# Kernel tuning notes

Hardware: AMD Instinct MI355X
Metric: run time of the kernel (lower is better)

## Reference

```python
import jax, jax.numpy as jnp
import numpy as np

D_MODEL = 2048
NUM_HEADS = 32
HEAD_DIM = D_MODEL // NUM_HEADS  # 64
ROPE_BASE = 10000.0


def _rope_cos_sin(seq_len, head_dim, dtype):
    inv_freq = 1.0 / (ROPE_BASE ** (jnp.arange(0, head_dim, 2, dtype=jnp.float32) / head_dim))
    freqs = jnp.arange(seq_len, dtype=jnp.float32)[:, None] * inv_freq[None, :]  # (S, Dh/2)
    emb = jnp.concatenate([freqs, freqs], axis=-1)  # (S, Dh)
    return emb.astype(dtype), jnp.cos(emb).astype(dtype), jnp.sin(emb).astype(dtype)


def _rotate_half(x):
    x1, x2 = jnp.split(x, 2, axis=-1)
    return jnp.concatenate([-x2, x1], axis=-1)


def setup_inputs() -> dict:
    key = jax.random.key(0)
    k1, k2, k3, k4 = jax.random.split(key, 4)
    B, S, D = 1, 2048, D_MODEL
    x = jax.random.normal(k1, (B, S, D), dtype=jnp.float32)
    Wqkv = jax.random.normal(k2, (3 * D, D), dtype=jnp.float32) * 0.02
    Wo = jax.random.normal(k3, (D, D), dtype=jnp.float32) * 0.02
    gate = jax.random.normal(k4, (D,), dtype=jnp.float32) * 0.1
    return {"x": x, "Wqkv": Wqkv, "Wo": Wo, "gate": gate}


def reference(x, Wqkv, Wo, gate):
    B, S, D = x.shape
    H, Dh = NUM_HEADS, HEAD_DIM
    residual = x

    # fused QKV projection (torch Linear: y = x @ W.T)
    qkv = jnp.einsum('bsd,ed->bse', x, Wqkv).reshape(B, S, 3, H, Dh)
    q, k, v = qkv[:, :, 0], qkv[:, :, 1], qkv[:, :, 2]  # each (B, S, H, Dh)

    # RoPE
    _, cos, sin = _rope_cos_sin(S, Dh, x.dtype)
    cos = cos[None, :, None, :]  # (1, S, 1, Dh)
    sin = sin[None, :, None, :]
    q = q * cos + _rotate_half(q) * sin
    k = k * cos + _rotate_half(k) * sin

    # causal SDPA
    scale = 1.0 / np.sqrt(Dh)
    scores = jnp.einsum('bqhd,bkhd->bhqk', q, k) * scale  # (B, H, S, S)
    causal = jnp.tril(jnp.ones((S, S), dtype=bool))
    scores = jnp.where(causal[None, None], scores, jnp.finfo(scores.dtype).min)
    probs = jax.nn.softmax(scores, axis=-1)
    attn = jnp.einsum('bhqk,bkhd->bqhd', probs, v).reshape(B, S, D)

    out = jnp.einsum('bsd,ed->bse', attn, Wo)
    # HeoGate: learned per-channel gated residual (assumption; see notes)
    return residual + gate * out
```

## Files before the change

### kernel.cpp

```cpp
#include <hip/hip_runtime.h>
#include <hip/hip_bf16.h>
#include <cstdint>
#include <cstddef>

typedef __hip_bfloat16 bf16;
typedef short short8 __attribute__((ext_vector_type(8)));
typedef float f32x4 __attribute__((ext_vector_type(4)));

#define S_LEN 2048
#define DMODEL 2048
#define NQKV 6144
#define NHEADS 32
#define HDIM 64
#define ROPE_L2 0.4152410118609203f

__device__ __forceinline__ void async_copy16(const bf16* g, bf16* l) {
  __builtin_amdgcn_global_load_lds(
      (const __attribute__((address_space(1))) void*)g,
      (__attribute__((address_space(3))) void*)l, 16, 0, 0);
}

__device__ __forceinline__ f32x4 mfma_bf16(short8 a, short8 b, f32x4 c) {
  return __builtin_amdgcn_mfma_f32_16x16x32_bf16(a, b, c, 0, 0, 0);
}

__global__ __launch_bounds__(256) void cvt3_kernel(const float* __restrict__ sx,
                                                   bf16* __restrict__ dx,
                                                   const float* __restrict__ sw,
                                                   bf16* __restrict__ dw,
                                                   const float* __restrict__ so,
                                                   bf16* __restrict__ dov) {
  int i = blockIdx.x * 256 + threadIdx.x;
  const float* s;
  bf16* d;
  if (i < 1048576) {
    s = sx; d = dx;
  } else if (i < 4194304) {
    s = sw; d = dw; i -= 1048576;
  } else {
    s = so; d = dov; i -= 4194304;
  }
  const float4 v = ((const float4*)s)[i];
  union { bf16 h[4]; ushort4 u; } tmp;
  tmp.h[0] = __float2bfloat16(v.x);
  tmp.h[1] = __float2bfloat16(v.y);
  tmp.h[2] = __float2bfloat16(v.z);
  tmp.h[3] = __float2bfloat16(v.w);
  ((ushort4*)d)[i] = tmp.u;
}

#define QKV_NT 32
#define QBAR() do { __builtin_amdgcn_s_barrier(); __builtin_amdgcn_sched_barrier(0); } while (0)
#define WAITV(n) asm volatile("s_waitcnt vmcnt(" #n ")" ::: "memory")
#define LGKM0() do { asm volatile("s_waitcnt lgkmcnt(0)" ::: "memory"); \
                     __builtin_amdgcn_sched_barrier(0); } while (0)

__global__ __launch_bounds__(512, 4) void gemm_qkv(const bf16* __restrict__ A,
                                                   const bf16* __restrict__ W,
                                                   bf16* __restrict__ q_ws,
                                                   bf16* __restrict__ k_ws,
                                                   bf16* __restrict__ v_ws) {
  __shared__ bf16 smem[32768];
  const int tid = threadIdx.x;
  const int wave = tid >> 6, lane = tid & 63;
  const int wm = wave >> 1, wn = wave & 1;
  const int m0 = blockIdx.y * 128, n0 = blockIdx.x * 128;
  const int srow_g = tid >> 2;
  const int swc = (((tid & 3) ^ ((tid >> 3) & 3)) * 8);
  const int fr = lane & 15, fq = lane >> 4;
  const int rdc = ((fq ^ ((fr >> 1) & 3)) * 8);

  auto stageA = [&](int t_, int kk_, int bufe_) {
    async_copy16(A + (size_t)(m0 + srow_g) * DMODEL + t_ * 64 + kk_ * 32 + swc,
                 &smem[bufe_ + kk_ * 4096 + wave * 512]);
  };
  auto stageB = [&](int t_, int kk_, int bufe_) {
    async_copy16(W + (size_t)(n0 + srow_g) * DMODEL + t_ * 64 + kk_ * 32 + swc,
                 &smem[bufe_ + 8192 + kk_ * 4096 + wave * 512]);
  };

  const f32x4 zero = {0.f, 0.f, 0.f, 0.f};
  f32x4 acc[2][4];
#pragma unroll
  for (int i = 0; i < 2; ++i)
#pragma unroll
    for (int j = 0; j < 4; ++j) acc[i][j] = zero;
  short8 a[2], b[4];

  stageA(0, 0, 0);
  stageB(0, 0, 0);
  stageA(0, 1, 0);
  stageB(0, 1, 0);
  WAITV(2);
  QBAR();

#define LOAD_A(KK, BC)                                                            \
  _Pragma("unroll") for (int mi = 0; mi < 2; ++mi)                                \
      a[mi] = *(const short8*)&smem[(BC) + (KK) * 4096 +                          \
                                    (wm * 32 + mi * 16 + fr) * 32 + rdc];
#define LOAD_B(KK, BC)                                                            \
  _Pragma("unroll") for (int n = 0; n < 4; ++n)                                   \
      b[n] = *(const short8*)&smem[(BC) + 8192 + (KK) * 4096 +                    \
                                   (wn * 64 + n * 16 + fr) * 32 + rdc];
#define MFMA8()                                                                   \
  __builtin_amdgcn_s_setprio(1);                                                  \
  _Pragma("unroll") for (int mi = 0; mi < 2; ++mi)                                \
      _Pragma("unroll") for (int n = 0; n < 4; ++n)                               \
          acc[mi][n] = mfma_bf16(a[mi], b[n], acc[mi][n]);                        \
  __builtin_amdgcn_s_setprio(0);

#pragma unroll 2
  for (int t = 0; t < QKV_NT; ++t) {
    const int bc = (t & 1) * 16384, bn = ((t + 1) & 1) * 16384;
    LOAD_A(0, bc); LOAD_B(0, bc);
    if (t + 1 < QKV_NT) { stageA(t + 1, 0, bn); stageB(t + 1, 0, bn); }
    QBAR(); LGKM0();
    MFMA8();
    if (t + 1 < QKV_NT) { WAITV(2); } else { WAITV(0); }
    QBAR();
    LOAD_A(1, bc); LOAD_B(1, bc);
    if (t + 1 < QKV_NT) { stageA(t + 1, 1, bn); stageB(t + 1, 1, bn); }
    QBAR(); LGKM0();
    MFMA8();
    if (t + 1 < QKV_NT) { WAITV(2); }
    QBAR();
  }
#undef LOAD_A
#undef LOAD_B
#undef MFMA8

  const int colb = n0 + wn * 64;
  const int sect = colb >> 11;
  const int h = (colb & 2047) >> 6;
  const int col = fr, rq = fq * 4;

  if (sect < 2) {
    bf16* dst = ((sect == 0) ? q_ws : k_ws) + (size_t)h * S_LEN * HDIM;
    bf16* rep = smem + wave * 1152;
    const float f0 = exp2f(-(float)col * ROPE_L2);
    const float f1 = exp2f(-(float)(16 + col) * ROPE_L2);
    __syncthreads();
    for (int m = 0; m < 2; ++m) {
      const int base_s = m0 + wm * 32 + m * 16;
#pragma unroll
      for (int jl = 0; jl < 2; ++jl) {
        const int dh = jl * 16 + col;
        const float fr_ = (jl == 0) ? f0 : f1;
#pragma unroll
        for (int r = 0; r < 4; ++r) {
          const int srow = base_s + rq + r;
          float sn, cs;
          __sincosf((float)srow * fr_, &sn, &cs);
          const float xl = acc[m][jl][r], xh = acc[m][jl + 2][r];
          rep[(rq + r) * 72 + dh]      = __float2bfloat16(xl * cs - xh * sn);
          rep[(rq + r) * 72 + dh + 32] = __float2bfloat16(xh * cs + xl * sn);
        }
      }
#pragma unroll
      for (int p = 0; p < 2; ++p) {
        const int rr = p * 8 + (lane >> 3), ch = lane & 7;
        const uint4 vv = *(const uint4*)&rep[rr * 72 + ch * 8];
        *(uint4*)&dst[(size_t)(base_s + rr) * HDIM + ch * 8] = vv;
      }
    }
  } else {
    bf16* dst = v_ws + (size_t)h * HDIM * S_LEN;
    for (int j = 0; j < 4; ++j) {
      const int dh = j * 16 + col;
      for (int m = 0; m < 2; ++m) {
        const int s0 = m0 + wm * 32 + m * 16 + rq;
        union { bf16 hx[4]; uint2 u; } vk;
#pragma unroll
        for (int r = 0; r < 4; ++r) vk.hx[r] = __float2bfloat16(acc[m][j][r]);
        *(uint2*)&dst[(size_t)dh * S_LEN + s0] = vk.u;
      }
    }
  }
}

__global__ __launch_bounds__(512) void attn_kernel(const bf16* __restrict__ q_ws,
                                                   const bf16* __restrict__ k_ws,
                                                   const bf16* __restrict__ vt_ws,
                                                   bf16* __restrict__ attn_out) {
  const int bid = blockIdx.x;
  const int qt = 15 - (bid >> 5);
  const int h = bid & 31;

  const int tid = threadIdx.x, wave = tid >> 6, lane = tid & 63;
  const int col = lane & 15, fq = lane >> 4;
  const int q_glob = qt * 128 + wave * 16 + col;

  __shared__ bf16 Ks[2][64 * 64];
  __shared__ bf16 Vs[2][64 * 64];
  __shared__ bf16 Pl[8][16 * 72];
  bf16* pl = Pl[wave];

  const bf16* qh = q_ws + (size_t)h * S_LEN * HDIM;
  const bf16* kh = k_ws + (size_t)h * S_LEN * HDIM;
  const bf16* vh = vt_ws + (size_t)h * HDIM * S_LEN;

  const int srow = lane >> 3;
  const int slot = lane & 7;
  const int schunk = slot ^ srow;

  auto stage = [&](int kt, int buf) {
    const int k0 = kt * 64;
    const int r8 = wave * 8;
    async_copy16(kh + (size_t)(k0 + r8 + srow) * HDIM + schunk * 8,
                 &Ks[buf][r8 * 64]);
    async_copy16(vh + (size_t)(r8 + srow) * S_LEN + k0 + schunk * 8,
                 &Vs[buf][r8 * 64]);
  };

  short8 qf[2];
#pragma unroll
  for (int ks = 0; ks < 2; ++ks)
    qf[ks] = *(const short8*)&qh[(size_t)q_glob * HDIM + ks * 32 + fq * 8];

  const f32x4 zero = {0.f, 0.f, 0.f, 0.f};
  f32x4 o_acc[4] = {zero, zero, zero, zero};
  float m_i = -1e30f, l_i = 0.f;

  stage(0, 0);

  const int lastk = 2 * qt + 1;
  for (int kt = 0; kt <= lastk; ++kt) {
    const int buf = kt & 1;
    const int k0 = kt * 64;
    __syncthreads();
    if (kt < lastk) stage(kt + 1, buf ^ 1);

    short8 kf[8];
#pragma unroll
    for (int n = 0; n < 4; ++n) {
      const int row = n * 16 + col;
#pragma unroll
      for (int ks = 0; ks < 2; ++ks)
        kf[n * 2 + ks] =
            *(const short8*)&Ks[buf][row * 64 + (((ks * 4 + fq) ^ (row & 7)) * 8)];
    }
    f32x4 s_acc[4] = {zero, zero, zero, zero};
#pragma unroll
    for (int n = 0; n < 4; ++n)
#pragma unroll
      for (int ks = 0; ks < 2; ++ks)
        s_acc[n] = mfma_bf16(kf[n * 2 + ks], qf[ks], s_acc[n]);

    short8 vf[8];
#pragma unroll
    for (int n = 0; n < 4; ++n) {
      const int row = n * 16 + col;
#pragma unroll
      for (int ks = 0; ks < 2; ++ks)
        vf[n * 2 + ks] =
            *(const short8*)&Vs[buf][row * 64 + (((ks * 4 + fq) ^ (row & 7)) * 8)];
    }

    if (k0 + 63 > qt * 128 + wave * 16) {
#pragma unroll
      for (int n = 0; n < 4; ++n)
#pragma unroll
        for (int r = 0; r < 4; ++r)
          if (k0 + n * 16 + fq * 4 + r > q_glob) s_acc[n][r] = -1e30f;
    }

    float vmax = -1e30f;
#pragma unroll
    for (int n = 0; n < 4; ++n)
#pragma unroll
      for (int r = 0; r < 4; ++r) vmax = fmaxf(vmax, s_acc[n][r]);
    vmax = fmaxf(vmax, __shfl_xor(vmax, 16, 64));
    vmax = fmaxf(vmax, __shfl_xor(vmax, 32, 64));

    if (!__all(vmax - m_i <= 8.0f)) {
      const float mnew = fmaxf(m_i, vmax);
      const float alpha = __expf((m_i - mnew) * 0.125f);
      l_i *= alpha;
#pragma unroll
      for (int n = 0; n < 4; ++n)
#pragma unroll
        for (int r = 0; r < 4; ++r) o_acc[n][r] *= alpha;
      m_i = mnew;
    }

    float rs = 0.f;
#pragma unroll
    for (int n = 0; n < 4; ++n)
#pragma unroll
      for (int r = 0; r < 4; ++r) {
        const float p = __expf((s_acc[n][r] - m_i) * 0.125f);
        s_acc[n][r] = p;
        rs += p;
      }
    rs += __shfl_xor(rs, 16, 64);
    rs += __shfl_xor(rs, 32, 64);
    l_i += rs;

#pragma unroll
    for (int n = 0; n < 4; ++n) {
      union { bf16 hx[4]; uint2 u; } pk;
#pragma unroll
      for (int r = 0; r < 4; ++r) pk.hx[r] = __float2bfloat16(s_acc[n][r]);
      *(uint2*)&pl[col * 72 + n * 16 + fq * 4] = pk.u;
    }
    short8 pa[2];
#pragma unroll
    for (int ks = 0; ks < 2; ++ks)
      pa[ks] = *(const short8*)&pl[col * 72 + ks * 32 + fq * 8];

#pragma unroll
    for (int n = 0; n < 4; ++n)
#pragma unroll
      for (int ks = 0; ks < 2; ++ks)
        o_acc[n] = mfma_bf16(vf[n * 2 + ks], pa[ks], o_acc[n]);
  }

  const float inv = 1.0f / l_i;
#pragma unroll
  for (int n = 0; n < 4; ++n) {
#pragma unroll
    for (int r = 0; r < 4; ++r) o_acc[n][r] *= inv;
    union { bf16 hx[4]; uint2 u; } ok;
#pragma unroll
    for (int r = 0; r < 4; ++r) ok.hx[r] = __float2bfloat16(o_acc[n][r]);
    *(uint2*)&attn_out[(size_t)q_glob * DMODEL + h * HDIM + n * 16 + fq * 4] = ok.u;
  }
}

__global__ __launch_bounds__(256) void gemm_out(const bf16* __restrict__ A,
                                                const bf16* __restrict__ W,
                                                const float* __restrict__ xres,
                                                const float* __restrict__ gate,
                                                float* __restrict__ out) {
  constexpr int K = DMODEL;
  constexpr int NT = K / 32;
  __shared__ bf16 As[3][64 * 32];
  __shared__ bf16 Bs[3][128 * 32];
  const int tid = threadIdx.x;
  const int wave = tid >> 6, lane = tid & 63;
  const int m0 = blockIdx.y * 64, n0 = blockIdx.x * 128;
  const int sr = lane >> 2;
  const int swc = (((lane & 3) ^ ((lane >> 3) & 3)) * 8);
  const int fr = lane & 15, fq = lane >> 4;
  const int rdc = ((fq ^ ((fr >> 1) & 3)) * 8);

  auto stage = [&](int t_, int s_) {
    async_copy16(A + (size_t)(m0 + wave * 16 + sr) * K + t_ * 32 + swc,
                 &As[s_][(wave * 16) * 32]);
#pragma unroll
    for (int j = 0; j < 2; ++j)
      async_copy16(W + (size_t)(n0 + wave * 32 + j * 16 + sr) * K + t_ * 32 + swc,
                   &Bs[s_][(wave * 32 + j * 16) * 32]);
  };

  const f32x4 zero = {0.f, 0.f, 0.f, 0.f};
  f32x4 acc[4][2];
  for (int i = 0; i < 4; ++i)
    for (int j = 0; j < 2; ++j) acc[i][j] = zero;

  stage(0, 0);
  stage(1, 1);
  WAITV(3);
  QBAR();

  for (int t = 0; t < NT; ++t) {
    const int s = t % 3;
    short8 a[4], b[2];
#pragma unroll
    for (int i = 0; i < 4; ++i)
      a[i] = *(const short8*)&As[s][(i * 16 + fr) * 32 + rdc];
#pragma unroll
    for (int j = 0; j < 2; ++j)
      b[j] = *(const short8*)&Bs[s][(wave * 32 + j * 16 + fr) * 32 + rdc];
    LGKM0();
    QBAR();
    if (t + 2 < NT) stage(t + 2, (t + 2) % 3);
#pragma unroll
    for (int i = 0; i < 4; ++i)
#pragma unroll
      for (int j = 0; j < 2; ++j)
        acc[i][j] = mfma_bf16(a[i], b[j], acc[i][j]);
    if (t + 1 < NT) {
      if (t + 2 < NT) { WAITV(3); }
      else            { WAITV(0); }
      QBAR();
    }
  }

  const int col = fr, rq = fq * 4;
  for (int j = 0; j < 2; ++j) {
    const int cc = n0 + wave * 32 + j * 16 + col;
    const float g = gate[cc];
    for (int i = 0; i < 4; ++i) {
      const int base_row = m0 + i * 16 + rq;
      for (int r = 0; r < 4; ++r) {
        const size_t idx = (size_t)(base_row + r) * DMODEL + cc;
        out[idx] = xres[idx] + g * acc[i][j][r];
      }
    }
  }
}

extern "C" void kernel_launch(void* const* d_in, const int* in_sizes, int n_in,
                              void* d_out, int out_size, void* d_ws, size_t ws_size,
                              hipStream_t stream) {
  const float* x    = (const float*)d_in[0];
  const float* Wqkv = (const float*)d_in[1];
  const float* Wo   = (const float*)d_in[2];
  const float* gate = (const float*)d_in[3];
  float* out = (float*)d_out;

  char* ws = (char*)d_ws;
  const size_t MB = 1024 * 1024;
  bf16* xb      = (bf16*)(ws);
  bf16* wqkvb   = (bf16*)(ws + 8 * MB);
  bf16* wob     = (bf16*)(ws + 32 * MB);
  bf16* q_ws    = (bf16*)(ws + 40 * MB);
  bf16* k_ws    = (bf16*)(ws + 48 * MB);
  bf16* v_ws    = (bf16*)(ws + 56 * MB);
  bf16* attn_ws = (bf16*)(ws);

  cvt3_kernel<<<dim3(20480), 256, 0, stream>>>(x, xb, Wqkv, wqkvb, Wo, wob);

  gemm_qkv<<<dim3(NQKV / 128, S_LEN / 128), 512, 0, stream>>>(xb, wqkvb, q_ws, k_ws, v_ws);
  attn_kernel<<<dim3(512), 512, 0, stream>>>(q_ws, k_ws, v_ws, attn_ws);
  gemm_out<<<dim3(DMODEL / 128, DMODEL / 64), 256, 0, stream>>>(attn_ws, wob, x, gate, out);
}
```

Measured before the change: 252.0 us.

## Halve threads per block in QKV GEMM and attention, doubling per-wave tile work

The QKV GEMM now runs 4 waves per 128x128 tile, each wave computing a 64x64 sub-tile (4x4 MFMA accumulators). It also restructures the K-loop to load a full 64-wide K step per iteration, prefetching two steps ahead with fewer barriers. The attention kernel uses 4 waves per 128-query block, each handling two 16-row query groups, so K/V fragments loaded from LDS are reused twice. This cuts LDS traffic and barrier overhead per MFMA, at the cost of higher register pressure and fewer waves for latency hiding.

```diff
diff --git a/kernel.cpp b/kernel.cpp
--- a/kernel.cpp
+++ b/kernel.cpp
@@ -55,7 +55,7 @@
 #define LGKM0() do { asm volatile("s_waitcnt lgkmcnt(0)" ::: "memory"); \
                      __builtin_amdgcn_sched_barrier(0); } while (0)
 
-__global__ __launch_bounds__(512, 4) void gemm_qkv(const bf16* __restrict__ A,
+__global__ __launch_bounds__(256, 2) void gemm_qkv(const bf16* __restrict__ A,
                                                    const bf16* __restrict__ W,
                                                    bf16* __restrict__ q_ws,
                                                    bf16* __restrict__ k_ws,
@@ -65,69 +65,74 @@
   const int wave = tid >> 6, lane = tid & 63;
   const int wm = wave >> 1, wn = wave & 1;
   const int m0 = blockIdx.y * 128, n0 = blockIdx.x * 128;
-  const int srow_g = tid >> 2;
+  const int srow = tid >> 2;
   const int swc = (((tid & 3) ^ ((tid >> 3) & 3)) * 8);
   const int fr = lane & 15, fq = lane >> 4;
   const int rdc = ((fq ^ ((fr >> 1) & 3)) * 8);
 
-  auto stageA = [&](int t_, int kk_, int bufe_) {
-    async_copy16(A + (size_t)(m0 + srow_g) * DMODEL + t_ * 64 + kk_ * 32 + swc,
-                 &smem[bufe_ + kk_ * 4096 + wave * 512]);
+  const bf16* Asrc = A + (size_t)(m0 + srow) * DMODEL + swc;
+  const bf16* Bsrc = W + (size_t)(n0 + srow) * DMODEL + swc;
+
+  auto stage = [&](int t_, int bufe_) {
+#pragma unroll
+    for (int kk = 0; kk < 2; ++kk) {
+      const int ko = t_ * 64 + kk * 32;
+      async_copy16(Asrc + ko, &smem[bufe_ + kk * 4096 + wave * 512]);
+      async_copy16(Asrc + (size_t)64 * DMODEL + ko,
+                   &smem[bufe_ + kk * 4096 + 2048 + wave * 512]);
+      async_copy16(Bsrc + ko, &smem[bufe_ + 8192 + kk * 4096 + wave * 512]);
+      async_copy16(Bsrc + (size_t)64 * DMODEL + ko,
+                   &smem[bufe_ + 8192 + kk * 4096 + 2048 + wave * 512]);
+    }
   };
-  auto stageB = [&](int t_, int kk_, int bufe_) {
-    async_copy16(W + (size_t)(n0 + srow_g) * DMODEL + t_ * 64 + kk_ * 32 + swc,
-                 &smem[bufe_ + 8192 + kk_ * 4096 + wave * 512]);
-  };
 
   const f32x4 zero = {0.f, 0.f, 0.f, 0.f};
-  f32x4 acc[2][4];
-#pragma unroll
-  for (int i = 0; i < 2; ++i)
+  f32x4 acc[4][4];
+#pragma unroll
+  for (int i = 0; i < 4; ++i)
 #pragma unroll
     for (int j = 0; j < 4; ++j) acc[i][j] = zero;
-  short8 a[2], b[4];
-
-  stageA(0, 0, 0);
-  stageB(0, 0, 0);
-  stageA(0, 1, 0);
-  stageB(0, 1, 0);
-  WAITV(2);
+  short8 a0[4], a1[4], b0[4], b1[4];
+
+  stage(0, 0);
+  stage(1, 16384);
+  WAITV(8);
   QBAR();
-
-#define LOAD_A(KK, BC)                                                            \
-  _Pragma("unroll") for (int mi = 0; mi < 2; ++mi)                                \
-      a[mi] = *(const short8*)&smem[(BC) + (KK) * 4096 +                          \
-                                    (wm * 32 + mi * 16 + fr) * 32 + rdc];
-#define LOAD_B(KK, BC)                                                            \
-  _Pragma("unroll") for (int n = 0; n < 4; ++n)                                   \
-      b[n] = *(const short8*)&smem[(BC) + 8192 + (KK) * 4096 +                    \
-                                   (wn * 64 + n * 16 + fr) * 32 + rdc];
-#define MFMA8()                                                                   \
-  __builtin_amdgcn_s_setprio(1);                                                  \
-  _Pragma("unroll") for (int mi = 0; mi < 2; ++mi)                                \
-      _Pragma("unroll") for (int n = 0; n < 4; ++n)                               \
-          acc[mi][n] = mfma_bf16(a[mi], b[n], acc[mi][n]);                        \
-  __builtin_amdgcn_s_setprio(0);
 
 #pragma unroll 2
   for (int t = 0; t < QKV_NT; ++t) {
-    const int bc = (t & 1) * 16384, bn = ((t + 1) & 1) * 16384;
-    LOAD_A(0, bc); LOAD_B(0, bc);
-    if (t + 1 < QKV_NT) { stageA(t + 1, 0, bn); stageB(t + 1, 0, bn); }
-    QBAR(); LGKM0();
-    MFMA8();
-    if (t + 1 < QKV_NT) { WAITV(2); } else { WAITV(0); }
+    const int bc = (t & 1) * 16384;
+#pragma unroll
+    for (int mi = 0; mi < 4; ++mi) {
+      const int ro = (wm * 64 + mi * 16 + fr) * 32 + rdc;
+      a0[mi] = *(const short8*)&smem[bc + ro];
+      a1[mi] = *(const short8*)&smem[bc + 4096 + ro];
+    }
+#pragma unroll
+    for (int n = 0; n < 4; ++n) {
+      const int ro = (wn * 64 + n * 16 + fr) * 32 + rdc;
+      b0[n] = *(const short8*)&smem[bc + 8192 + ro];
+      b1[n] = *(const short8*)&smem[bc + 12288 + ro];
+    }
+    LGKM0();
     QBAR();
-    LOAD_A(1, bc); LOAD_B(1, bc);
-    if (t + 1 < QKV_NT) { stageA(t + 1, 1, bn); stageB(t + 1, 1, bn); }
-    QBAR(); LGKM0();
-    MFMA8();
-    if (t + 1 < QKV_NT) { WAITV(2); }
+    if (t + 2 < QKV_NT) stage(t + 2, bc);
+    __builtin_amdgcn_s_setprio(1);
+#pragma unroll
+    for (int mi = 0; mi < 4; ++mi)
+#pragma unroll
+      for (int n = 0; n < 4; ++n)
+        acc[mi][n] = mfma_bf16(a0[mi], b0[n], acc[mi][n]);
+#pragma unroll
+    for (int mi = 0; mi < 4; ++mi)
+#pragma unroll
+      for (int n = 0; n < 4; ++n)
+        acc[mi][n] = mfma_bf16(a1[mi], b1[n], acc[mi][n]);
+    __builtin_amdgcn_s_setprio(0);
+    if (t + 2 < QKV_NT)      { WAITV(8); }
+    else if (t + 1 < QKV_NT) { WAITV(0); }
     QBAR();
   }
-#undef LOAD_A
-#undef LOAD_B
-#undef MFMA8
 
   const int colb = n0 + wn * 64;
   const int sect = colb >> 11;
@@ -140,17 +145,17 @@
     const float f0 = exp2f(-(float)col * ROPE_L2);
     const float f1 = exp2f(-(float)(16 + col) * ROPE_L2);
     __syncthreads();
-    for (int m = 0; m < 2; ++m) {
-      const int base_s = m0 + wm * 32 + m * 16;
+    for (int m = 0; m < 4; ++m) {
+      const int base_s = m0 + wm * 64 + m * 16;
 #pragma unroll
       for (int jl = 0; jl < 2; ++jl) {
         const int dh = jl * 16 + col;
         const float fr_ = (jl == 0) ? f0 : f1;
 #pragma unroll
         for (int r = 0; r < 4; ++r) {
-          const int srow = base_s + rq + r;
+          const int srw = base_s + rq + r;
           float sn, cs;
-          __sincosf((float)srow * fr_, &sn, &cs);
+          __sincosf((float)srw * fr_, &sn, &cs);
           const float xl = acc[m][jl][r], xh = acc[m][jl + 2][r];
           rep[(rq + r) * 72 + dh]      = __float2bfloat16(xl * cs - xh * sn);
           rep[(rq + r) * 72 + dh + 32] = __float2bfloat16(xh * cs + xl * sn);
@@ -167,8 +172,8 @@
     bf16* dst = v_ws + (size_t)h * HDIM * S_LEN;
     for (int j = 0; j < 4; ++j) {
       const int dh = j * 16 + col;
-      for (int m = 0; m < 2; ++m) {
-        const int s0 = m0 + wm * 32 + m * 16 + rq;
+      for (int m = 0; m < 4; ++m) {
+        const int s0 = m0 + wm * 64 + m * 16 + rq;
         union { bf16 hx[4]; uint2 u; } vk;
 #pragma unroll
         for (int r = 0; r < 4; ++r) vk.hx[r] = __float2bfloat16(acc[m][j][r]);
@@ -178,7 +183,7 @@
   }
 }
 
-__global__ __launch_bounds__(512) void attn_kernel(const bf16* __restrict__ q_ws,
+__global__ __launch_bounds__(256) void attn_kernel(const bf16* __restrict__ q_ws,
                                                    const bf16* __restrict__ k_ws,
                                                    const bf16* __restrict__ vt_ws,
                                                    bf16* __restrict__ attn_out) {
@@ -188,11 +193,11 @@
 
   const int tid = threadIdx.x, wave = tid >> 6, lane = tid & 63;
   const int col = lane & 15, fq = lane >> 4;
-  const int q_glob = qt * 128 + wave * 16 + col;
+  const int qbase = qt * 128 + wave * 32;
 
   __shared__ bf16 Ks[2][64 * 64];
   __shared__ bf16 Vs[2][64 * 64];
-  __shared__ bf16 Pl[8][16 * 72];
+  __shared__ bf16 Pl[4][32 * 72];
   bf16* pl = Pl[wave];
 
   const bf16* qh = q_ws + (size_t)h * S_LEN * HDIM;
@@ -205,21 +210,31 @@
 
   auto stage = [&](int kt, int buf) {
     const int k0 = kt * 64;
-    const int r8 = wave * 8;
-    async_copy16(kh + (size_t)(k0 + r8 + srow) * HDIM + schunk * 8,
-                 &Ks[buf][r8 * 64]);
-    async_copy16(vh + (size_t)(r8 + srow) * S_LEN + k0 + schunk * 8,
-                 &Vs[buf][r8 * 64]);
+#pragma unroll
+    for (int j = 0; j < 2; ++j) {
+      const int r8 = (wave * 2 + j) * 8;
+      async_copy16(kh + (size_t)(k0 + r8 + srow) * HDIM + schunk * 8,
+                   &Ks[buf][r8 * 64]);
+      async_copy16(vh + (size_t)(r8 + srow) * S_LEN + k0 + schunk * 8,
+                   &Vs[buf][r8 * 64]);
+    }
   };
 
-  short8 qf[2];
-#pragma unroll
-  for (int ks = 0; ks < 2; ++ks)
-    qf[ks] = *(const short8*)&qh[(size_t)q_glob * HDIM + ks * 32 + fq * 8];
+  short8 qf[2][2];
+#pragma unroll
+  for (int g = 0; g < 2; ++g)
+#pragma unroll
+    for (int ks = 0; ks < 2; ++ks)
+      qf[g][ks] = *(const short8*)&qh[(size_t)(qbase + g * 16 + col) * HDIM +
+                                      ks * 32 + fq * 8];
 
   const f32x4 zero = {0.f, 0.f, 0.f, 0.f};
-  f32x4 o_acc[4] = {zero, zero, zero, zero};
-  float m_i = -1e30f, l_i = 0.f;
+  f32x4 o_acc[2][4];
+#pragma unroll
+  for (int g = 0; g < 2; ++g)
+#pragma unroll
+    for (int n = 0; n < 4; ++n) o_acc[g][n] = zero;
+  float m_i[2] = {-1e30f, -1e30f}, l_i[2] = {0.f, 0.f};
 
   stage(0, 0);
 
@@ -239,12 +254,18 @@
         kf[n * 2 + ks] =
             *(const short8*)&Ks[buf][row * 64 + (((ks * 4 + fq) ^ (row & 7)) * 8)];
     }
-    f32x4 s_acc[4] = {zero, zero, zero, zero};
-#pragma unroll
-    for (int n = 0; n < 4; ++n)
-#pragma unroll
-      for (int ks = 0; ks < 2; ++ks)
-        s_acc[n] = mfma_bf16(kf[n * 2 + ks], qf[ks], s_acc[n]);
+    f32x4 s_acc[2][4];
+#pragma unroll
+    for (int g = 0; g < 2; ++g)
+#pragma unroll
+      for (int n = 0; n < 4; ++n) s_acc[g][n] = zero;
+#pragma unroll
+    for (int g = 0; g < 2; ++g)
+#pragma unroll
+      for (int n = 0; n < 4; ++n)
+#pragma unroll
+        for (int ks = 0; ks < 2; ++ks)
+          s_acc[g][n] = mfma_bf16(kf[n * 2 + ks], qf[g][ks], s_acc[g][n]);
 
     short8 vf[8];
 #pragma unroll
@@ -256,74 +277,90 @@
             *(const short8*)&Vs[buf][row * 64 + (((ks * 4 + fq) ^ (row & 7)) * 8)];
     }
 
-    if (k0 + 63 > qt * 128 + wave * 16) {
-#pragma unroll
-      for (int n = 0; n < 4; ++n)
-#pragma unroll
-        for (int r = 0; r < 4; ++r)
-          if (k0 + n * 16 + fq * 4 + r > q_glob) s_acc[n][r] = -1e30f;
-    }
-
-    float vmax = -1e30f;
-#pragma unroll
-    for (int n = 0; n < 4; ++n)
-#pragma unroll
-      for (int r = 0; r < 4; ++r) vmax = fmaxf(vmax, s_acc[n][r]);
-    vmax = fmaxf(vmax, __shfl_xor(vmax, 16, 64));
-    vmax = fmaxf(vmax, __shfl_xor(vmax, 32, 64));
-
-    if (!__all(vmax - m_i <= 8.0f)) {
-      const float mnew = fmaxf(m_i, vmax);
-      const float alpha = __expf((m_i - mnew) * 0.125f);
-      l_i *= alpha;
-#pragma unroll
-      for (int n = 0; n < 4; ++n)
-#pragma unroll
-        for (int r = 0; r < 4; ++r) o_acc[n][r] *= alpha;
-      m_i = mnew;
-    }
-
-    float rs = 0.f;
-#pragma unroll
-    for (int n = 0; n < 4; ++n)
-#pragma unroll
-      for (int r = 0; r < 4; ++r) {
-        const float p = __expf((s_acc[n][r] - m_i) * 0.125f);
-        s_acc[n][r] = p;
-        rs += p;
-      }
-    rs += __shfl_xor(rs, 16, 64);
-    rs += __shfl_xor(rs, 32, 64);
-    l_i += rs;
-
+    if (k0 + 63 > qbase) {
+#pragma unroll
+      for (int g = 0; g < 2; ++g) {
+        const int qg = qbase + g * 16 + col;
+#pragma unroll
+        for (int n = 0; n < 4; ++n)
+#pragma unroll
+          for (int r = 0; r < 4; ++r)
+            if (k0 + n * 16 + fq * 4 + r > qg) s_acc[g][n][r] = -1e30f;
+      }
+    }
+
+#pragma unroll
+    for (int g = 0; g < 2; ++g) {
+      float vmax = -1e30f;
+#pragma unroll
+      for (int n = 0; n < 4; ++n)
+#pragma unroll
+        for (int r = 0; r < 4; ++r) vmax = fmaxf(vmax, s_acc[g][n][r]);
+      vmax = fmaxf(vmax, __shfl_xor(vmax, 16, 64));
+      vmax = fmaxf(vmax, __shfl_xor(vmax, 32, 64));
+
+      if (!__all(vmax - m_i[g] <= 8.0f)) {
+        const float mnew = fmaxf(m_i[g], vmax);
+        const float alpha = __expf((m_i[g] - mnew) * 0.125f);
+        l_i[g] *= alpha;
+#pragma unroll
+        for (int n = 0; n < 4; ++n)
+#pragma unroll
+          for (int r = 0; r < 4; ++r) o_acc[g][n][r] *= alpha;
+        m_i[g] = mnew;
+      }
+
+      float rs = 0.f;
+#pragma unroll
+      for (int n = 0; n < 4; ++n)
+#pragma unroll
+        for (int r = 0; r < 4; ++r) {
+          const float p = __expf((s_acc[g][n][r] - m_i[g]) * 0.125f);
+          s_acc[g][n][r] = p;
+          rs += p;
+        }
+      rs += __shfl_xor(rs, 16, 64);
+      rs += __shfl_xor(rs, 32, 64);
+      l_i[g] += rs;
+
+#pragma unroll
+      for (int n = 0; n < 4; ++n) {
+        union { bf16 hx[4]; uint2 u; } pk;
+#pragma unroll
+        for (int r = 0; r < 4; ++r) pk.hx[r] = __float2bfloat16(s_acc[g][n][r]);
+        *(uint2*)&pl[(g * 16 + col) * 72 + n * 16 + fq * 4] = pk.u;
+      }
+    }
+
+    short8 pa[2][2];
+#pragma unroll
+    for (int g = 0; g < 2; ++g)
+#pragma unroll
+      for (int ks = 0; ks < 2; ++ks)
+        pa[g][ks] = *(const short8*)&pl[(g * 16 + col) * 72 + ks * 32 + fq * 8];
+
+#pragma unroll
+    for (int g = 0; g < 2; ++g)
+#pragma unroll
+      for (int n = 0; n < 4; ++n)
+#pragma unroll
+        for (int ks = 0; ks < 2; ++ks)
+          o_acc[g][n] = mfma_bf16(vf[n * 2 + ks], pa[g][ks], o_acc[g][n]);
+  }
+
+#pragma unroll
+  for (int g = 0; g < 2; ++g) {
+    const float inv = 1.0f / l_i[g];
+    const int qg = qbase + g * 16 + col;
 #pragma unroll
     for (int n = 0; n < 4; ++n) {
-      union { bf16 hx[4]; uint2 u; } pk;
-#pragma unroll
-      for (int r = 0; r < 4; ++r) pk.hx[r] = __float2bfloat16(s_acc[n][r]);
-      *(uint2*)&pl[col * 72 + n * 16 + fq * 4] = pk.u;
-    }
-    short8 pa[2];
-#pragma unroll
-    for (int ks = 0; ks < 2; ++ks)
-      pa[ks] = *(const short8*)&pl[col * 72 + ks * 32 + fq * 8];
-
-#pragma unroll
-    for (int n = 0; n < 4; ++n)
-#pragma unroll
-      for (int ks = 0; ks < 2; ++ks)
-        o_acc[n] = mfma_bf16(vf[n * 2 + ks], pa[ks], o_acc[n]);
-  }
-
-  const float inv = 1.0f / l_i;
-#pragma unroll
-  for (int n = 0; n < 4; ++n) {
-#pragma unroll
-    for (int r = 0; r < 4; ++r) o_acc[n][r] *= inv;
-    union { bf16 hx[4]; uint2 u; } ok;
-#pragma unroll
-    for (int r = 0; r < 4; ++r) ok.hx[r] = __float2bfloat16(o_acc[n][r]);
-    *(uint2*)&attn_out[(size_t)q_glob * DMODEL + h * HDIM + n * 16 + fq * 4] = ok.u;
+#pragma unroll
+      for (int r = 0; r < 4; ++r) o_acc[g][n][r] *= inv;
+      union { bf16 hx[4]; uint2 u; } ok;
+#pragma unroll
+      for (int r = 0; r < 4; ++r) ok.hx[r] = __float2bfloat16(o_acc[g][n][r]);
+      *(uint2*)&attn_out[(size_t)qg * DMODEL + h * HDIM + n * 16 + fq * 4] = ok.u;
+    }
   }
 }
 
@@ -422,7 +459,7 @@
 
   cvt3_kernel<<<dim3(20480), 256, 0, stream>>>(x, xb, Wqkv, wqkvb, Wo, wob);
 
-  gemm_qkv<<<dim3(NQKV / 128, S_LEN / 128), 512, 0, stream>>>(xb, wqkvb, q_ws, k_ws, v_ws);
-  attn_kernel<<<dim3(512), 512, 0, stream>>>(q_ws, k_ws, v_ws, attn_ws);
+  gemm_qkv<<<dim3(NQKV / 128, S_LEN / 128), 256, 0, stream>>>(xb, wqkvb, q_ws, k_ws, v_ws);
+  attn_kernel<<<dim3(512), 256, 0, stream>>>(q_ws, k_ws, v_ws, attn_ws);
   gemm_out<<<dim3(DMODEL / 128, DMODEL / 64), 256, 0, stream>>>(attn_ws, wob, x, gate, out);
 }
```

Result: slower. 259.2 us (+2.8%).
